# Optimization experiments

Hardware: AMD Instinct MI355X
Metric: run time of the kernel (lower is better)

The kernel has to match this reference:

```python
import jax, jax.numpy as jnp
import numpy as np

B, E, D_IN, D_OUT = 16384, 64, 128, 128
ES = 3


def _orthogonal_centroids(key, num_experts, in_features):
    # Mirrors get_orthogonal_vectors: E//2 orthonormal vectors, concat with negatives.
    g = jax.random.normal(key, (in_features, num_experts // 2), dtype=jnp.float32)
    q, _ = jnp.linalg.qr(g)              # [in, E//2], orthonormal columns
    v = q.T                              # [E//2, in]
    return jnp.concatenate([v, -v], axis=0)  # [E, in]


def setup_inputs() -> dict:
    key = jax.random.key(0)
    kx, kc, kw = jax.random.split(key, 3)
    x = jax.random.normal(kx, (B, D_IN), dtype=jnp.float32)
    d_scale = jnp.full((1, 1, 1), 0.1, dtype=jnp.float32)  # nn.Parameter([[[0.1]]])
    centroids = _orthogonal_centroids(kc, E, D_IN)          # buffer, [E, in]
    # Per-expert Linear(in, out) params, fan-in scaled like torch default.
    W = jax.random.normal(kw, (E, D_IN, D_OUT), dtype=jnp.float32) / np.sqrt(D_IN)
    b = jnp.zeros((E, D_OUT), dtype=jnp.float32)
    return {"x": x, "d_scale": d_scale, "centroids": centroids, "W": W, "b": b, "es": ES}


def reference(x, d_scale, centroids, W, b, es):
    # scaled_diff: [B, E, D]; d_scale is a scalar param broadcast as [1,1,1]
    scaled_diff = d_scale * (x[:, None, :] - centroids[None, :, :])
    distance_sq = jnp.mean(scaled_diff * scaled_diff, axis=2)          # [B, E]
    # picked = es nearest centroids (argsort ascending, take first es)
    _, picked = jax.lax.top_k(-distance_sq, es)                        # [B, es] int32
    # NOTE: faithful to source quirk — weights use the FIRST es columns of
    # distance_sq (distance_sq[:, :es]), NOT the distances of picked experts.
    select_distances = distance_sq[:, :es]                             # [B, es]
    select_weights = 1.0 / (1.0 + select_distances)
    select_weights = select_weights / jnp.sum(select_weights, axis=1, keepdims=True)
    # Dense-all-experts then gather (clean jit-able baseline for the irregular
    # gather-compute-scatter the torch code does per unique expert).
    y_all = jnp.einsum('bi,eio->beo', x, W) + b[None, :, :]            # [B, E, out]
    expert_out = jnp.take_along_axis(y_all, picked[:, :, None], axis=1)  # [B, es, out]
    return jnp.sum(expert_out * select_weights[:, :, None], axis=1)    # [B, out]
```

## Files before the change

### kernel.cpp

```cpp
#include <hip/hip_runtime.h>
#include <hip/hip_bf16.h>

#define NB   16384
#define NE   64
#define DIN  128
#define DOUT 128
#define CPAD 32

#define WS_COUNTS   0
#define WS_CURSOR   2048
#define WS_BASE     4096
#define WS_NWORK    4160
#define WS_WORK     4224
#define WS_PICKED   8192
#define WS_PW       57344
#define WS_PAIRROW  106496
#define WS_PAIRW    155648
#define WS_PAIRP    204800
#define WS_SLOT     253952
#define WS_WH       6545408
#define WS_WL       7069696
#define WS_END      7593984
#define MAX_WORK    832

typedef __attribute__((ext_vector_type(8))) short short8v;
typedef __attribute__((ext_vector_type(4))) float f32x4;

static __device__ __forceinline__ short f2bf(float f) {
  unsigned u = __float_as_uint(f);
  unsigned r = (u + 0x7fffu + ((u >> 16) & 1u)) >> 16;
  return (short)r;
}
static __device__ __forceinline__ float bf2f(short s) {
  return __uint_as_float(((unsigned)(unsigned short)s) << 16);
}

__global__ __launch_bounds__(64) void k0_init(int* __restrict__ wsI) {
  if (threadIdx.x < NE) wsI[WS_COUNTS + threadIdx.x * CPAD] = 0;
}

__global__ __launch_bounds__(256) void k1_route(
    const float* __restrict__ x, const float* __restrict__ dsc,
    const float* __restrict__ cent, float* __restrict__ out,
    int* __restrict__ wsI, float* __restrict__ wsF, int zero_out) {
  __shared__ float cl[NE][132];
  __shared__ float xl[16][132];
  __shared__ float dl[4][64];
  const int tid = threadIdx.x;
  const int row0 = blockIdx.x * 16;

  const float4* c4 = (const float4*)cent;
  #pragma unroll
  for (int k = 0; k < 8; ++k) {
    int idx = tid + k * 256;
    int e = idx >> 5, dc = idx & 31;
    *(float4*)&cl[e][dc * 4] = c4[idx];
  }
  const float4* x4 = (const float4*)x + row0 * 32;
  #pragma unroll
  for (int k = 0; k < 2; ++k) {
    int idx = tid + k * 256;
    int r = idx >> 5, dc = idx & 31;
    *(float4*)&xl[r][dc * 4] = x4[idx];
  }
  if (zero_out) {
    float4* o4 = (float4*)out + row0 * 32;
    float4 z; z.x = z.y = z.z = z.w = 0.f;
    #pragma unroll
    for (int k = 0; k < 2; ++k) o4[tid + k * 256] = z;
  }
  __syncthreads();

  const int lane = tid & 63, wv = tid >> 6;
  const float ds = dsc[0];

  for (int rr = wv; rr < 16; rr += 4) {
    float4 r0 = {0.f, 0.f, 0.f, 0.f}, r1 = {0.f, 0.f, 0.f, 0.f};
    {
      #pragma clang fp contract(off)
      for (int i = 0; i < 16; ++i) {
        float4 xa = *(const float4*)&xl[rr][i * 8];
        float4 xb = *(const float4*)&xl[rr][i * 8 + 4];
        float4 ca = *(const float4*)&cl[lane][i * 8];
        float4 cb = *(const float4*)&cl[lane][i * 8 + 4];
        float t0 = ds * (xa.x - ca.x), t1 = ds * (xa.y - ca.y);
        float t2 = ds * (xa.z - ca.z), t3 = ds * (xa.w - ca.w);
        float u0 = ds * (xb.x - cb.x), u1 = ds * (xb.y - cb.y);
        float u2 = ds * (xb.z - cb.z), u3 = ds * (xb.w - cb.w);
        r0.x += t0 * t0; r0.y += t1 * t1; r0.z += t2 * t2; r0.w += t3 * t3;
        r1.x += u0 * u0; r1.y += u1 * u1; r1.z += u2 * u2; r1.w += u3 * u3;
      }
    }
    float s = ((r0.x + r0.y) + (r0.z + r0.w)) + ((r1.x + r1.y) + (r1.z + r1.w));
    float dist = s / 128.0f;

    dl[wv][lane] = dist;
    int rank = 0;
    #pragma unroll
    for (int j = 0; j < 64; j += 8) {
      float4 da = *(const float4*)&dl[wv][j];
      float4 db = *(const float4*)&dl[wv][j + 4];
      rank += (da.x < dist || (da.x == dist && (j + 0) < lane)) ? 1 : 0;
      rank += (da.y < dist || (da.y == dist && (j + 1) < lane)) ? 1 : 0;
      rank += (da.z < dist || (da.z == dist && (j + 2) < lane)) ? 1 : 0;
      rank += (da.w < dist || (da.w == dist && (j + 3) < lane)) ? 1 : 0;
      rank += (db.x < dist || (db.x == dist && (j + 4) < lane)) ? 1 : 0;
      rank += (db.y < dist || (db.y == dist && (j + 5) < lane)) ? 1 : 0;
      rank += (db.z < dist || (db.z == dist && (j + 6) < lane)) ? 1 : 0;
      rank += (db.w < dist || (db.w == dist && (j + 7) < lane)) ? 1 : 0;
    }
    unsigned long long m0 = __ballot(rank == 0);
    unsigned long long m1 = __ballot(rank == 1);
    unsigned long long m2 = __ballot(rank == 2);
    int i0 = __ffsll(m0) - 1;
    int i1 = __ffsll(m1) - 1;
    int i2 = __ffsll(m2) - 1;

    float d0 = dl[wv][0], d1 = dl[wv][1], d2 = dl[wv][2];
    float w0 = 1.f / (1.f + d0), w1 = 1.f / (1.f + d1), w2 = 1.f / (1.f + d2);
    float sw = (w0 + w1) + w2;
    w0 /= sw; w1 /= sw; w2 /= sw;

    int row = row0 + rr;
    if (lane < 3) {
      float w = (lane == 0) ? w0 : ((lane == 1) ? w1 : w2);
      int p = (lane == 0) ? i0 : ((lane == 1) ? i1 : i2);
      wsI[WS_PICKED + row * 3 + lane] = p;
      wsF[WS_PW + row * 3 + lane] = w;
    }
  }
}

__global__ __launch_bounds__(256) void k1b_count(int* __restrict__ wsI) {
  __shared__ int h[NE];
  const int tid = threadIdx.x;
  if (tid < NE) h[tid] = 0;
  __syncthreads();
  for (int i = blockIdx.x * 256 + tid; i < 3 * NB; i += 64 * 256)
    atomicAdd(&h[wsI[WS_PICKED + i]], 1);
  __syncthreads();
  if (tid < NE && h[tid]) atomicAdd(&wsI[WS_COUNTS + tid * CPAD], h[tid]);
}

__global__ __launch_bounds__(64) void k2_scan(int* __restrict__ wsI) {
  const int lane = threadIdx.x;
  int cnt = wsI[WS_COUNTS + lane * CPAD];
  int xs = cnt;
  #pragma unroll
  for (int off = 1; off < 64; off <<= 1) {
    int y = __shfl_up(xs, off, 64);
    if (lane >= off) xs += y;
  }
  int excl = xs - cnt;
  wsI[WS_BASE + lane] = excl;
  wsI[WS_CURSOR + lane * CPAD] = excl;
  int nt = (cnt + 63) >> 6;
  int ts = nt;
  #pragma unroll
  for (int off = 1; off < 64; off <<= 1) {
    int y = __shfl_up(ts, off, 64);
    if (lane >= off) ts += y;
  }
  int texcl = ts - nt;
  for (int t = 0; t < nt; ++t) wsI[WS_WORK + texcl + t] = (lane << 16) | t;
  if (lane == 63) wsI[WS_NWORK] = ts;
}

__global__ __launch_bounds__(256) void k3_scatter(int* __restrict__ wsI,
                                                  float* __restrict__ wsF) {
  int p = blockIdx.x * 256 + threadIdx.x;
  if (p < 3 * NB) {
    int e = wsI[WS_PICKED + p];
    float w = wsF[WS_PW + p];
    int pos = atomicAdd(&wsI[WS_CURSOR + e * CPAD], 1);
    wsI[WS_PAIRROW + pos] = p / 3;
    wsI[WS_PAIRP + pos]   = p;
    wsF[WS_PAIRW + pos]   = w;
  }
}

__global__ __launch_bounds__(256) void k_wsplit(const float* __restrict__ W,
                                                short* __restrict__ gwh,
                                                short* __restrict__ gwl) {
  __shared__ float T[DOUT][68];
  const int e = blockIdx.x >> 1, kh = blockIdx.x & 1;
  const int tid = threadIdx.x;
  const float4* Wg = (const float4*)(W + (long)e * DIN * DOUT);

  #pragma unroll
  for (int k = 0; k < 8; ++k) {
    int idx = tid + k * 256;
    int dl = idx >> 5, o4 = idx & 31;
    float4 v = Wg[(long)(64 * kh + dl) * 32 + o4];
    T[4 * o4 + 0][dl] = v.x;
    T[4 * o4 + 1][dl] = v.y;
    T[4 * o4 + 2][dl] = v.z;
    T[4 * o4 + 3][dl] = v.w;
  }
  __syncthreads();

  #pragma unroll
  for (int it = 0; it < 4; ++it) {
    int task = tid + it * 256;
    int o = task >> 3, dc = task & 7;
    const float* tp = &T[o][8 * dc];
    short8v wh, wl;
    #pragma unroll
    for (int i = 0; i < 8; ++i) {
      float f = tp[i];
      short h = f2bf(f);
      wh[i] = h;
      wl[i] = f2bf(f - bf2f(h));
    }
    long base = ((long)e * DOUT + o) * DIN + 64 * kh + 8 * dc;
    *(short8v*)&gwh[base] = wh;
    *(short8v*)&gwl[base] = wl;
  }
}

__global__ __launch_bounds__(256) void k4_mfma(
    const float* __restrict__ x, const short* __restrict__ gwh,
    const short* __restrict__ gwl, const float* __restrict__ bias,
    const int* __restrict__ wsI, const float* __restrict__ wsF,
    float* __restrict__ dst) {
  __shared__ float biasl[DOUT];
  __shared__ int   rowsl[64];
  __shared__ int   pl[64];
  __shared__ float wgt[64];

  const int nwork = wsI[WS_NWORK];
  const int bid = blockIdx.x;
  if (bid >= nwork) return;
  const int wk = wsI[WS_WORK + bid];
  const int e = wk >> 16, t = wk & 0xffff;
  const int cnt = wsI[WS_COUNTS + e * CPAD];
  const int srcb = wsI[WS_BASE + e] + t * 64;
  const int m = min(64, cnt - t * 64);
  const int tid = threadIdx.x;
  const int lane = tid & 63, wv = tid >> 6;
  const int l15 = lane & 15, kg = lane >> 4;

  if (tid < 64) {
    int src = srcb + ((tid < m) ? tid : 0);
    rowsl[tid] = wsI[WS_PAIRROW + src];
    pl[tid]    = wsI[WS_PAIRP + src];
    wgt[tid]   = (tid < m) ? wsF[WS_PAIRW + srcb + tid] : 0.f;
  }
  if (tid < DOUT) biasl[tid] = bias[e * DOUT + tid];
  __syncthreads();

  const float* xr = x + (long)rowsl[16 * wv + l15] * DIN + 8 * kg;
  short8v ah[4], al[4];
  #pragma unroll
  for (int s = 0; s < 4; ++s) {
    float4 fa = *(const float4*)(xr + 32 * s);
    float4 fb = *(const float4*)(xr + 32 * s + 4);
    float f[8] = {fa.x, fa.y, fa.z, fa.w, fb.x, fb.y, fb.z, fb.w};
    #pragma unroll
    for (int i = 0; i < 8; ++i) {
      short h = f2bf(f[i]);
      ah[s][i] = h;
      al[s][i] = f2bf(f[i] - bf2f(h));
    }
  }

  f32x4 acc[8];
  #pragma unroll
  for (int n = 0; n < 8; ++n) acc[n] = (f32x4){0.f, 0.f, 0.f, 0.f};

  const long ebase = (long)e * DOUT * DIN;
  #pragma unroll
  for (int n = 0; n < 8; ++n) {
    const long obase = ebase + (long)(16 * n + l15) * DIN + 8 * kg;
    #pragma unroll
    for (int s = 0; s < 4; ++s) {
      short8v bh = *(const short8v*)&gwh[obase + 32 * s];
      short8v bl = *(const short8v*)&gwl[obase + 32 * s];
      acc[n] = __builtin_amdgcn_mfma_f32_16x16x32_bf16(ah[s], bh, acc[n], 0, 0, 0);
      acc[n] = __builtin_amdgcn_mfma_f32_16x16x32_bf16(ah[s], bl, acc[n], 0, 0, 0);
      acc[n] = __builtin_amdgcn_mfma_f32_16x16x32_bf16(al[s], bh, acc[n], 0, 0, 0);
    }
  }

  #pragma unroll
  for (int j = 0; j < 4; ++j) {
    int r = 16 * wv + 4 * kg + j;
    if (r < m) {
      float w = wgt[r];
      #pragma unroll
      for (int n = 0; n < 8; ++n) {
        int o = 16 * n + l15;
        dst[(long)pl[r] * DOUT + o] = w * (acc[n][j] + biasl[o]);
      }
    }
  }
}

__global__ __launch_bounds__(256) void k4_f32(
    const float* __restrict__ x, const float* __restrict__ W,
    const float* __restrict__ bias, const int* __restrict__ wsI,
    const float* __restrict__ wsF, float* __restrict__ dst) {
  __shared__ float xT[DIN][68];
  __shared__ float Wl[32][DOUT];
  __shared__ int   rowsl[64];
  __shared__ float wl[64];

  const int nwork = wsI[WS_NWORK];
  const int bid = blockIdx.x;
  if (bid >= nwork) return;
  const int wk = wsI[WS_WORK + bid];
  const int e = wk >> 16, t = wk & 0xffff;
  const int cnt = wsI[WS_COUNTS + e * CPAD];
  const int srcb = wsI[WS_BASE + e] + t * 64;
  const int m = min(64, cnt - t * 64);
  const int tid = threadIdx.x;

  if (tid < 64) {
    int src = srcb + ((tid < m) ? tid : 0);
    rowsl[tid] = wsI[WS_PAIRROW + src];
    wl[tid] = (tid < m) ? wsF[WS_PAIRW + srcb + tid] : 0.f;
  }
  __syncthreads();
  {
    int r = tid >> 2;
    int d0 = (tid & 3) * 32;
    const float* xr = x + (long)rowsl[r] * DIN + d0;
    #pragma unroll
    for (int k = 0; k < 32; k += 4) {
      float4 v = *(const float4*)(xr + k);
      xT[d0 + k + 0][r] = v.x;
      xT[d0 + k + 1][r] = v.y;
      xT[d0 + k + 2][r] = v.z;
      xT[d0 + k + 3][r] = v.w;
    }
  }
  float acc[4][8];
  #pragma unroll
  for (int i = 0; i < 4; ++i)
    #pragma unroll
    for (int j = 0; j < 8; ++j) acc[i][j] = 0.f;
  const int tr = tid & 15, tc = tid >> 4;
  for (int dc = 0; dc < DIN; dc += 32) {
    __syncthreads();
    const float4* Wg = (const float4*)(W + (long)e * DIN * DOUT + dc * DOUT);
    float4* Wl4 = (float4*)&Wl[0][0];
    #pragma unroll
    for (int k = 0; k < 4; ++k) Wl4[tid + k * 256] = Wg[tid + k * 256];
    __syncthreads();
    #pragma unroll 8
    for (int dd = 0; dd < 32; ++dd) {
      float4 xv = *(const float4*)&xT[dc + dd][tr * 4];
      float4 wa = *(const float4*)&Wl[dd][tc * 8];
      float4 wb = *(const float4*)&Wl[dd][tc * 8 + 4];
      float xs[4] = {xv.x, xv.y, xv.z, xv.w};
      float ws8[8] = {wa.x, wa.y, wa.z, wa.w, wb.x, wb.y, wb.z, wb.w};
      #pragma unroll
      for (int i = 0; i < 4; ++i)
        #pragma unroll
        for (int j = 0; j < 8; ++j) acc[i][j] += xs[i] * ws8[j];
    }
  }
  #pragma unroll
  for (int i = 0; i < 4; ++i) {
    int r = tr * 4 + i;
    if (r < m) {
      int row = rowsl[r];
      float w = wl[r];
      float* op = dst + (long)row * DOUT + tc * 8;
      const float* bp = bias + (long)e * DOUT + tc * 8;
      #pragma unroll
      for (int j = 0; j < 8; ++j) atomicAdd(&op[j], w * (acc[i][j] + bp[j]));
    }
  }
}

__global__ __launch_bounds__(256) void k5_gather(const float* __restrict__ slot,
                                                 float* __restrict__ out) {
  int gid = blockIdx.x * 256 + threadIdx.x;
  int row = gid >> 5, c4 = gid & 31;
  const float4* s = (const float4*)(slot + (long)row * 3 * DOUT) + c4;
  float4 a = s[0], b = s[32], c = s[64];
  float4 o;
  o.x = (a.x + b.x) + c.x;
  o.y = (a.y + b.y) + c.y;
  o.z = (a.z + b.z) + c.z;
  o.w = (a.w + b.w) + c.w;
  ((float4*)out)[gid] = o;
}

extern "C" void kernel_launch(void* const* d_in, const int* in_sizes, int n_in,
                              void* d_out, int out_size, void* d_ws, size_t ws_size,
                              hipStream_t stream) {
  const float* x    = (const float*)d_in[0];
  const float* dsc  = (const float*)d_in[1];
  const float* cent = (const float*)d_in[2];
  const float* W    = (const float*)d_in[3];
  const float* bias = (const float*)d_in[4];
  float* out = (float*)d_out;
  int* wsI = (int*)d_ws;
  float* wsF = (float*)d_ws;

  const size_t need = (size_t)WS_END * 4;
  const int useSlot = (ws_size >= need) ? 1 : 0;

  hipLaunchKernelGGL(k0_init,    dim3(1),            dim3(64),  0, stream, wsI);
  hipLaunchKernelGGL(k1_route,   dim3(NB / 16),      dim3(256), 0, stream,
                     x, dsc, cent, out, wsI, wsF, useSlot ? 0 : 1);
  hipLaunchKernelGGL(k1b_count,  dim3(64),           dim3(256), 0, stream, wsI);
  hipLaunchKernelGGL(k2_scan,    dim3(1),            dim3(64),  0, stream, wsI);
  hipLaunchKernelGGL(k3_scatter, dim3(3 * NB / 256), dim3(256), 0, stream, wsI, wsF);
  if (useSlot) {
    float* slot = (float*)d_ws + WS_SLOT;
    short* gwh  = (short*)(wsI + WS_WH);
    short* gwl  = (short*)(wsI + WS_WL);
    hipLaunchKernelGGL(k_wsplit,  dim3(2 * NE),      dim3(256), 0, stream, W, gwh, gwl);
    hipLaunchKernelGGL(k4_mfma,   dim3(MAX_WORK),    dim3(256), 0, stream,
                       x, gwh, gwl, bias, wsI, wsF, slot);
    hipLaunchKernelGGL(k5_gather, dim3(NB * 32 / 256), dim3(256), 0, stream, slot, out);
  } else {
    hipLaunchKernelGGL(k4_f32,    dim3(MAX_WORK),    dim3(256), 0, stream,
                       x, W, bias, wsI, wsF, out);
  }
}
```

Before: 167.8 us.

## Replace global atomics with per-block histograms and block-aggregated scatter

Drops the init kernel. k1b_count now writes per-block histograms that k2_scan reduces, so no global atomic counts are needed. k3_scatter aggregates per-expert offsets in shared memory and issues one global atomic per expert per block instead of one per pair. The routing kernel now gives each wave four rows and reads x straight from global memory rather than staging it through LDS. These changes cut launch and atomic-contention overhead in the small routing stages. The main MFMA kernel is untouched, so the overall effect depends on how much time those small stages take.

```diff
diff --git a/kernel.cpp b/kernel.cpp
--- a/kernel.cpp
+++ b/kernel.cpp
@@ -12,15 +12,16 @@
 #define WS_BASE     4096
 #define WS_NWORK    4160
 #define WS_WORK     4224
-#define WS_PICKED   8192
-#define WS_PW       57344
-#define WS_PAIRROW  106496
-#define WS_PAIRW    155648
-#define WS_PAIRP    204800
-#define WS_SLOT     253952
-#define WS_WH       6545408
-#define WS_WL       7069696
-#define WS_END      7593984
+#define WS_HIST     5120
+#define WS_PICKED   9216
+#define WS_PW       58368
+#define WS_PAIRROW  107520
+#define WS_PAIRW    156672
+#define WS_PAIRP    205824
+#define WS_SLOT     254976
+#define WS_WH       6546432
+#define WS_WL       7070720
+#define WS_END      7595008
 #define MAX_WORK    832
 
 typedef __attribute__((ext_vector_type(8))) short short8v;
@@ -35,16 +36,11 @@
   return __uint_as_float(((unsigned)(unsigned short)s) << 16);
 }
 
-__global__ __launch_bounds__(64) void k0_init(int* __restrict__ wsI) {
-  if (threadIdx.x < NE) wsI[WS_COUNTS + threadIdx.x * CPAD] = 0;
-}
-
 __global__ __launch_bounds__(256) void k1_route(
     const float* __restrict__ x, const float* __restrict__ dsc,
-    const float* __restrict__ cent, float* __restrict__ out,
-    int* __restrict__ wsI, float* __restrict__ wsF, int zero_out) {
+    const float* __restrict__ cent,
+    int* __restrict__ wsI, float* __restrict__ wsF) {
   __shared__ float cl[NE][132];
-  __shared__ float xl[16][132];
   __shared__ float dl[4][64];
   const int tid = threadIdx.x;
   const int row0 = blockIdx.x * 16;
@@ -56,44 +52,50 @@
     int e = idx >> 5, dc = idx & 31;
     *(float4*)&cl[e][dc * 4] = c4[idx];
   }
-  const float4* x4 = (const float4*)x + row0 * 32;
-  #pragma unroll
-  for (int k = 0; k < 2; ++k) {
-    int idx = tid + k * 256;
-    int r = idx >> 5, dc = idx & 31;
-    *(float4*)&xl[r][dc * 4] = x4[idx];
-  }
-  if (zero_out) {
-    float4* o4 = (float4*)out + row0 * 32;
-    float4 z; z.x = z.y = z.z = z.w = 0.f;
-    #pragma unroll
-    for (int k = 0; k < 2; ++k) o4[tid + k * 256] = z;
-  }
   __syncthreads();
 
   const int lane = tid & 63, wv = tid >> 6;
   const float ds = dsc[0];
-
-  for (int rr = wv; rr < 16; rr += 4) {
-    float4 r0 = {0.f, 0.f, 0.f, 0.f}, r1 = {0.f, 0.f, 0.f, 0.f};
-    {
-      #pragma clang fp contract(off)
-      for (int i = 0; i < 16; ++i) {
-        float4 xa = *(const float4*)&xl[rr][i * 8];
-        float4 xb = *(const float4*)&xl[rr][i * 8 + 4];
-        float4 ca = *(const float4*)&cl[lane][i * 8];
-        float4 cb = *(const float4*)&cl[lane][i * 8 + 4];
+  const int rbase = row0 + 4 * wv;
+  const float* xr = x + (long)rbase * DIN;
+
+  float4 r0[4], r1[4];
+  #pragma unroll
+  for (int r = 0; r < 4; ++r) {
+    r0[r] = (float4){0.f, 0.f, 0.f, 0.f};
+    r1[r] = (float4){0.f, 0.f, 0.f, 0.f};
+  }
+  {
+    #pragma clang fp contract(off)
+    for (int i = 0; i < 16; ++i) {
+      float4 ca = *(const float4*)&cl[lane][i * 8];
+      float4 cb = *(const float4*)&cl[lane][i * 8 + 4];
+      #pragma unroll
+      for (int r = 0; r < 4; ++r) {
+        float4 xa = *(const float4*)(xr + r * DIN + i * 8);
+        float4 xb = *(const float4*)(xr + r * DIN + i * 8 + 4);
         float t0 = ds * (xa.x - ca.x), t1 = ds * (xa.y - ca.y);
         float t2 = ds * (xa.z - ca.z), t3 = ds * (xa.w - ca.w);
         float u0 = ds * (xb.x - cb.x), u1 = ds * (xb.y - cb.y);
         float u2 = ds * (xb.z - cb.z), u3 = ds * (xb.w - cb.w);
-        r0.x += t0 * t0; r0.y += t1 * t1; r0.z += t2 * t2; r0.w += t3 * t3;
-        r1.x += u0 * u0; r1.y += u1 * u1; r1.z += u2 * u2; r1.w += u3 * u3;
+        r0[r].x += t0 * t0; r0[r].y += t1 * t1;
+        r0[r].z += t2 * t2; r0[r].w += t3 * t3;
+        r1[r].x += u0 * u0; r1[r].y += u1 * u1;
+        r1[r].z += u2 * u2; r1[r].w += u3 * u3;
       }
     }
-    float s = ((r0.x + r0.y) + (r0.z + r0.w)) + ((r1.x + r1.y) + (r1.z + r1.w));
-    float dist = s / 128.0f;
-
+  }
+  float distr[4];
+  #pragma unroll
+  for (int r = 0; r < 4; ++r) {
+    float s = ((r0[r].x + r0[r].y) + (r0[r].z + r0[r].w)) +
+              ((r1[r].x + r1[r].y) + (r1[r].z + r1[r].w));
+    distr[r] = s / 128.0f;
+  }
+
+  #pragma unroll
+  for (int r = 0; r < 4; ++r) {
+    float dist = distr[r];
     dl[wv][lane] = dist;
     int rank = 0;
     #pragma unroll
@@ -121,7 +123,7 @@
     float sw = (w0 + w1) + w2;
     w0 /= sw; w1 /= sw; w2 /= sw;
 
-    int row = row0 + rr;
+    int row = rbase + r;
     if (lane < 3) {
       float w = (lane == 0) ? w0 : ((lane == 1) ? w1 : w2);
       int p = (lane == 0) ? i0 : ((lane == 1) ? i1 : i2);
@@ -136,15 +138,19 @@
   const int tid = threadIdx.x;
   if (tid < NE) h[tid] = 0;
   __syncthreads();
-  for (int i = blockIdx.x * 256 + tid; i < 3 * NB; i += 64 * 256)
-    atomicAdd(&h[wsI[WS_PICKED + i]], 1);
-  __syncthreads();
-  if (tid < NE && h[tid]) atomicAdd(&wsI[WS_COUNTS + tid * CPAD], h[tid]);
+  const int base = blockIdx.x * 768;
+  #pragma unroll
+  for (int k = 0; k < 3; ++k)
+    atomicAdd(&h[wsI[WS_PICKED + base + tid + k * 256]], 1);
+  __syncthreads();
+  if (tid < NE) wsI[WS_HIST + blockIdx.x * NE + tid] = h[tid];
 }
 
 __global__ __launch_bounds__(64) void k2_scan(int* __restrict__ wsI) {
   const int lane = threadIdx.x;
-  int cnt = wsI[WS_COUNTS + lane * CPAD];
+  int cnt = 0;
+  for (int b = 0; b < 64; ++b) cnt += wsI[WS_HIST + b * NE + lane];
+  wsI[WS_COUNTS + lane * CPAD] = cnt;
   int xs = cnt;
   #pragma unroll
   for (int off = 1; off < 64; off <<= 1) {
@@ -168,15 +174,23 @@
 
 __global__ __launch_bounds__(256) void k3_scatter(int* __restrict__ wsI,
                                                   float* __restrict__ wsF) {
-  int p = blockIdx.x * 256 + threadIdx.x;
-  if (p < 3 * NB) {
-    int e = wsI[WS_PICKED + p];
-    float w = wsF[WS_PW + p];
-    int pos = atomicAdd(&wsI[WS_CURSOR + e * CPAD], 1);
-    wsI[WS_PAIRROW + pos] = p / 3;
-    wsI[WS_PAIRP + pos]   = p;
-    wsF[WS_PAIRW + pos]   = w;
-  }
+  __shared__ int h[NE];
+  __shared__ int hbase[NE];
+  const int tid = threadIdx.x;
+  if (tid < NE) h[tid] = 0;
+  __syncthreads();
+  int p = blockIdx.x * 256 + tid;
+  int e = wsI[WS_PICKED + p];
+  float w = wsF[WS_PW + p];
+  int myofs = atomicAdd(&h[e], 1);
+  __syncthreads();
+  if (tid < NE && h[tid])
+    hbase[tid] = atomicAdd(&wsI[WS_CURSOR + tid * CPAD], h[tid]);
+  __syncthreads();
+  int pos = hbase[e] + myofs;
+  wsI[WS_PAIRROW + pos] = p / 3;
+  wsI[WS_PAIRP + pos]   = p;
+  wsF[WS_PAIRW + pos]   = w;
 }
 
 __global__ __launch_bounds__(256) void k_wsplit(const float* __restrict__ W,
@@ -296,6 +310,20 @@
   }
 }
 
+__global__ __launch_bounds__(256) void k5_gather(const float* __restrict__ slot,
+                                                 float* __restrict__ out) {
+  int gid = blockIdx.x * 256 + threadIdx.x;
+  int row = gid >> 5, c4 = gid & 31;
+  const float4* s = (const float4*)(slot + (long)row * 3 * DOUT) + c4;
+  float4 a = s[0], b = s[32], c = s[64];
+  float4 o;
+  o.x = (a.x + b.x) + c.x;
+  o.y = (a.y + b.y) + c.y;
+  o.z = (a.z + b.z) + c.z;
+  o.w = (a.w + b.w) + c.w;
+  ((float4*)out)[gid] = o;
+}
+
 __global__ __launch_bounds__(256) void k4_f32(
     const float* __restrict__ x, const float* __restrict__ W,
     const float* __restrict__ bias, const int* __restrict__ wsI,
@@ -304,7 +332,6 @@
   __shared__ float Wl[32][DOUT];
   __shared__ int   rowsl[64];
   __shared__ float wl[64];
-
   const int nwork = wsI[WS_NWORK];
   const int bid = blockIdx.x;
   if (bid >= nwork) return;
@@ -314,7 +341,6 @@
   const int srcb = wsI[WS_BASE + e] + t * 64;
   const int m = min(64, cnt - t * 64);
   const int tid = threadIdx.x;
-
   if (tid < 64) {
     int src = srcb + ((tid < m) ? tid : 0);
     rowsl[tid] = wsI[WS_PAIRROW + src];
@@ -324,10 +350,10 @@
   {
     int r = tid >> 2;
     int d0 = (tid & 3) * 32;
-    const float* xr = x + (long)rowsl[r] * DIN + d0;
+    const float* xrw = x + (long)rowsl[r] * DIN + d0;
     #pragma unroll
     for (int k = 0; k < 32; k += 4) {
-      float4 v = *(const float4*)(xr + k);
+      float4 v = *(const float4*)(xrw + k);
       xT[d0 + k + 0][r] = v.x;
       xT[d0 + k + 1][r] = v.y;
       xT[d0 + k + 2][r] = v.z;
@@ -374,18 +400,9 @@
   }
 }
 
-__global__ __launch_bounds__(256) void k5_gather(const float* __restrict__ slot,
-                                                 float* __restrict__ out) {
-  int gid = blockIdx.x * 256 + threadIdx.x;
-  int row = gid >> 5, c4 = gid & 31;
-  const float4* s = (const float4*)(slot + (long)row * 3 * DOUT) + c4;
-  float4 a = s[0], b = s[32], c = s[64];
-  float4 o;
-  o.x = (a.x + b.x) + c.x;
-  o.y = (a.y + b.y) + c.y;
-  o.z = (a.z + b.z) + c.z;
-  o.w = (a.w + b.w) + c.w;
-  ((float4*)out)[gid] = o;
+__global__ __launch_bounds__(256) void k_zero_out(float* __restrict__ out) {
+  float4 z; z.x = z.y = z.z = z.w = 0.f;
+  ((float4*)out)[blockIdx.x * 256 + threadIdx.x] = z;
 }
 
 extern "C" void kernel_launch(void* const* d_in, const int* in_sizes, int n_in,
@@ -403,9 +420,8 @@
   const size_t need = (size_t)WS_END * 4;
   const int useSlot = (ws_size >= need) ? 1 : 0;
 
-  hipLaunchKernelGGL(k0_init,    dim3(1),            dim3(64),  0, stream, wsI);
   hipLaunchKernelGGL(k1_route,   dim3(NB / 16),      dim3(256), 0, stream,
-                     x, dsc, cent, out, wsI, wsF, useSlot ? 0 : 1);
+                     x, dsc, cent, wsI, wsF);
   hipLaunchKernelGGL(k1b_count,  dim3(64),           dim3(256), 0, stream, wsI);
   hipLaunchKernelGGL(k2_scan,    dim3(1),            dim3(64),  0, stream, wsI);
   hipLaunchKernelGGL(k3_scatter, dim3(3 * NB / 256), dim3(256), 0, stream, wsI, wsF);
@@ -418,6 +434,7 @@
                        x, gwh, gwl, bias, wsI, wsF, slot);
     hipLaunchKernelGGL(k5_gather, dim3(NB * 32 / 256), dim3(256), 0, stream, slot, out);
   } else {
+    hipLaunchKernelGGL(k_zero_out, dim3(NB * 32 / 256), dim3(256), 0, stream, out);
     hipLaunchKernelGGL(k4_f32,    dim3(MAX_WORK),    dim3(256), 0, stream,
                        x, W, bias, wsI, wsF, out);
   }
```

Result: faster. 158.2 us (-5.7%).
